# Kernel tuning notes

Measured on AMD Instinct MI355X. Metric: run time of the kernel, lower is better.

## Reference

```python
import jax, jax.numpy as jnp
import numpy as np

N_NODES = 50000
N_EDGES = 800000
D = 128
N_LAYERS = 6  # nbaselayer=3 -> branches of depth 1,2,3
NBASELAYER = 3
BN_EPS = 1e-5


def setup_inputs() -> dict:
    key = jax.random.key(0)
    ks = jax.random.split(key, 11)
    stdv = 1.0 / np.sqrt(D)
    return {
        "x": jax.random.normal(ks[0], (N_NODES, D), jnp.float32),
        "row": jax.random.randint(ks[1], (N_EDGES,), 0, N_NODES),
        "col": jax.random.randint(ks[2], (N_EDGES,), 0, N_NODES),
        "edge_weight": jax.random.uniform(ks[3], (N_EDGES,), jnp.float32),
        "W": jax.random.uniform(ks[4], (N_LAYERS, D, D), jnp.float32, -stdv, stdv),
        "SW": jax.random.uniform(ks[5], (N_LAYERS, D, D), jnp.float32, -stdv, stdv),
        "b": jax.random.uniform(ks[6], (N_LAYERS, D), jnp.float32, -stdv, stdv),
        "gamma": jax.random.uniform(ks[7], (N_LAYERS, D), jnp.float32, 0.5, 1.5),
        "beta": jax.random.normal(ks[8], (N_LAYERS, D), jnp.float32) * 0.1,
        "rmean": jax.random.normal(ks[9], (N_LAYERS, D), jnp.float32) * 0.1,
        "rvar": jax.random.uniform(ks[10], (N_LAYERS, D), jnp.float32, 0.5, 1.5),
    }


def reference(x, row, col, edge_weight, W, SW, b, gamma, beta, rmean, rvar):
    n = x.shape[0]

    def gcn(l, h):
        # dense GEMM: [N, D] @ [D, D]
        support = h @ W[l]
        # sparse aggregation (spmm): out[row] += w * support[col]
        msg = support[col] * edge_weight[:, None]  # [E, D]
        agg = jax.ops.segment_sum(msg, row, num_segments=n)
        # self-loop + bias
        out = agg + h @ SW[l] + b[l]
        # BatchNorm1d (eval mode: running stats)
        out = (out - rmean[l]) * jax.lax.rsqrt(rvar[l] + BN_EPS) * gamma[l] + beta[l]
        return jax.nn.relu(out)

    idx = 0
    for j in range(NBASELAYER):
        subx = x
        for _ in range(j + 1):
            # faithful to source: each inner layer consumes x (not subx)
            subx = gcn(idx, x)
            idx += 1
        x = x + subx  # aggrmethod='add'
    return x
```

## Files before the change

kernel.cpp:

```cpp
#include <hip/hip_runtime.h>

#define DD 128
#define NNODES 50000
#define NEDGES 800000
#define BN_EPS 1e-5f
#define NB1 ((NEDGES + 4095) / 4096)
#define NGROUPS ((NNODES + 255) / 256)

typedef float f32x4 __attribute__((ext_vector_type(4)));
typedef short bf16x8 __attribute__((ext_vector_type(8)));

__device__ __forceinline__ unsigned short f2bf(float f) {
    unsigned u = __float_as_uint(f);
    u = (u + 0x7FFFu + ((u >> 16) & 1u)) >> 16;
    return (unsigned short)u;
}
__device__ __forceinline__ float bf2f(unsigned short s) {
    return __uint_as_float((unsigned)s << 16);
}
__device__ __forceinline__ unsigned packbf(float a, float b) {
    return (unsigned)f2bf(a) | ((unsigned)f2bf(b) << 16);
}
__device__ __forceinline__ float lo_bf(unsigned u) { return __uint_as_float(u << 16); }
__device__ __forceinline__ float hi_bf(unsigned u) { return __uint_as_float(u & 0xFFFF0000u); }

__global__ __launch_bounds__(256) void count_convx_kernel(
    const int* __restrict__ row, int* __restrict__ pbase,
    const float* __restrict__ x, unsigned* __restrict__ h16u,
    int nedges, int npairs)
{
    const int bid = blockIdx.x;
    if (bid < NB1) {
        __shared__ int cnt[256];
        cnt[threadIdx.x] = 0;
        __syncthreads();
        const int estart = bid * 4096;
        const int eend = min(estart + 4096, nedges);
        for (int e = estart + threadIdx.x; e < eend; e += 256)
            atomicAdd(&cnt[row[e] >> 8], 1);
        __syncthreads();
        pbase[bid * 256 + threadIdx.x] = cnt[threadIdx.x];
    } else {
        int stride = (gridDim.x - NB1) * 256;
        for (int i = (bid - NB1) * 256 + threadIdx.x; i < npairs; i += stride) {
            float2 v = ((const float2*)x)[i];
            h16u[i] = packbf(v.x, v.y);
        }
    }
}

__global__ __launch_bounds__(256) void scanall_convwf_kernel(
    int* __restrict__ pbase, int* __restrict__ bktbase, int* __restrict__ rowptr,
    const float* __restrict__ W, const float* __restrict__ SW,
    unsigned short* __restrict__ Wf)
{
    if (blockIdx.x == 0) {
        __shared__ int buf[256];
        const int t = threadIdx.x;
        int s = 0;
#pragma unroll 4
        for (int blk = 0; blk < NB1; ++blk) {
            int tmp = pbase[blk * 256 + t];
            pbase[blk * 256 + t] = s;
            s += tmp;
        }
        const int v = s;
        buf[t] = v;
        __syncthreads();
#pragma unroll
        for (int off = 1; off < 256; off <<= 1) {
            int tv = (t >= off) ? buf[t - off] : 0;
            __syncthreads();
            buf[t] += tv;
            __syncthreads();
        }
        bktbase[t] = buf[t] - v;
        if (t == 255) bktbase[256] = buf[255];
        if (t == 0) rowptr[NNODES] = NEDGES;
        return;
    }
    int t = (blockIdx.x - 1) * 256 + threadIdx.x;
    if (t < 3 * 8 * 8 * 64) {
        int lane = t & 63;
        int nt   = (t >> 6) & 7;
        int ks   = (t >> 9) & 7;
        int li   = t >> 12;
        const int lmap[3] = {0, 2, 5};
        int l = lmap[li];
        int nn = nt * 16 + (lane & 15);
        unsigned short* dst = Wf + (((size_t)li * 64 + ks * 8 + nt) * 64 + lane) * 8;
#pragma unroll
        for (int i = 0; i < 8; ++i) {
            int k = ks * 32 + (lane >> 4) * 8 + i;
            float v = (k < 128) ? W[((size_t)l * 128 + k) * 128 + nn]
                                : SW[((size_t)l * 128 + (k - 128)) * 128 + nn];
            dst[i] = f2bf(v);
        }
    }
}

__global__ __launch_bounds__(256) void sort_pass1_kernel(
    const int* __restrict__ row, const int* __restrict__ col,
    const float* __restrict__ ew, const int* __restrict__ pbase,
    const int* __restrict__ bktbase, uint2* __restrict__ inter, int nedges)
{
    __shared__ int base[256];
    __shared__ int cnt[256];
    base[threadIdx.x] = pbase[blockIdx.x * 256 + threadIdx.x] + bktbase[threadIdx.x];
    cnt[threadIdx.x] = 0;
    __syncthreads();
    const int estart = blockIdx.x * 4096;
    const int eend = min(estart + 4096, nedges);
    for (int e = estart + threadIdx.x; e < eend; e += 256) {
        int r = row[e];
        int b = r >> 8;
        int k = atomicAdd(&cnt[b], 1);
        unsigned payload = (unsigned)col[e] | ((unsigned)f2bf(ew[e]) << 16);
        inter[base[b] + k] = make_uint2(payload, (unsigned)(r & 255));
    }
}

__global__ __launch_bounds__(256) void sort_pass2_kernel(
    const int* __restrict__ bktbase, const uint2* __restrict__ inter,
    int* __restrict__ rowptr, unsigned* __restrict__ cedge, int n)
{
    __shared__ int cnt[256];
    __shared__ int cur[256];
    const int g = blockIdx.x;
    const int rows0 = g * 256;
    const int jbeg = bktbase[g];
    const int jend = bktbase[g + 1];
    cnt[threadIdx.x] = 0;
    __syncthreads();
    for (int j = jbeg + threadIdx.x; j < jend; j += 256)
        atomicAdd(&cnt[inter[j].y], 1);
    __syncthreads();
    const int v = cnt[threadIdx.x];
    __syncthreads();
#pragma unroll
    for (int off = 1; off < 256; off <<= 1) {
        int t = (threadIdx.x >= off) ? cnt[threadIdx.x - off] : 0;
        __syncthreads();
        cnt[threadIdx.x] += t;
        __syncthreads();
    }
    const int rp = jbeg + cnt[threadIdx.x] - v;
    if (rows0 + threadIdx.x < n) rowptr[rows0 + threadIdx.x] = rp;
    cur[threadIdx.x] = rp;
    __syncthreads();
    for (int j = jbeg + threadIdx.x; j < jend; j += 256) {
        uint2 rec = inter[j];
        int p = atomicAdd(&cur[rec.y], 1);
        cedge[p] = rec.x;
    }
}

__global__ __launch_bounds__(256) void spmm_gather16_kernel(
    const uint4* __restrict__ h4, const int* __restrict__ rowptr,
    const unsigned* __restrict__ ce, uint4* __restrict__ agg4, int n)
{
    int node = blockIdx.x * 4 + (threadIdx.x >> 6);
    if (node >= n) return;
    const int lane = threadIdx.x & 63;
    const int q    = lane >> 4;
    const int l16  = lane & 15;
    const int beg = rowptr[node];
    const int end = rowptr[node + 1];

    float a0 = 0.f, a1 = 0.f, a2 = 0.f, a3 = 0.f;
    float a4 = 0.f, a5 = 0.f, a6 = 0.f, a7 = 0.f;

    int j = beg + q;
    for (; j + 12 < end; j += 16) {
        unsigned e0 = ce[j], e1 = ce[j+4], e2 = ce[j+8], e3 = ce[j+12];
        uint4 v0 = h4[(size_t)(e0 & 0xFFFFu) * 16 + l16];
        uint4 v1 = h4[(size_t)(e1 & 0xFFFFu) * 16 + l16];
        uint4 v2 = h4[(size_t)(e2 & 0xFFFFu) * 16 + l16];
        uint4 v3 = h4[(size_t)(e3 & 0xFFFFu) * 16 + l16];
        float w0 = bf2f((unsigned short)(e0 >> 16));
        float w1 = bf2f((unsigned short)(e1 >> 16));
        float w2 = bf2f((unsigned short)(e2 >> 16));
        float w3 = bf2f((unsigned short)(e3 >> 16));
        a0 += w0*lo_bf(v0.x) + w1*lo_bf(v1.x) + w2*lo_bf(v2.x) + w3*lo_bf(v3.x);
        a1 += w0*hi_bf(v0.x) + w1*hi_bf(v1.x) + w2*hi_bf(v2.x) + w3*hi_bf(v3.x);
        a2 += w0*lo_bf(v0.y) + w1*lo_bf(v1.y) + w2*lo_bf(v2.y) + w3*lo_bf(v3.y);
        a3 += w0*hi_bf(v0.y) + w1*hi_bf(v1.y) + w2*hi_bf(v2.y) + w3*hi_bf(v3.y);
        a4 += w0*lo_bf(v0.z) + w1*lo_bf(v1.z) + w2*lo_bf(v2.z) + w3*lo_bf(v3.z);
        a5 += w0*hi_bf(v0.z) + w1*hi_bf(v1.z) + w2*hi_bf(v2.z) + w3*hi_bf(v3.z);
        a6 += w0*lo_bf(v0.w) + w1*lo_bf(v1.w) + w2*lo_bf(v2.w) + w3*lo_bf(v3.w);
        a7 += w0*hi_bf(v0.w) + w1*hi_bf(v1.w) + w2*hi_bf(v2.w) + w3*hi_bf(v3.w);
    }
    for (; j < end; j += 4) {
        unsigned e = ce[j];
        uint4 v = h4[(size_t)(e & 0xFFFFu) * 16 + l16];
        float w = bf2f((unsigned short)(e >> 16));
        a0 += w * lo_bf(v.x); a1 += w * hi_bf(v.x);
        a2 += w * lo_bf(v.y); a3 += w * hi_bf(v.y);
        a4 += w * lo_bf(v.z); a5 += w * hi_bf(v.z);
        a6 += w * lo_bf(v.w); a7 += w * hi_bf(v.w);
    }
#pragma unroll
    for (int off = 16; off <= 32; off <<= 1) {
        a0 += __shfl_xor(a0, off); a1 += __shfl_xor(a1, off);
        a2 += __shfl_xor(a2, off); a3 += __shfl_xor(a3, off);
        a4 += __shfl_xor(a4, off); a5 += __shfl_xor(a5, off);
        a6 += __shfl_xor(a6, off); a7 += __shfl_xor(a7, off);
    }
    if (q == 0)
        agg4[(size_t)node * 16 + l16] =
            make_uint4(packbf(a0, a1), packbf(a2, a3), packbf(a4, a5), packbf(a6, a7));
}

__global__ __launch_bounds__(256) void gemm_mfma_kernel(
    unsigned short* __restrict__ h16,
    const unsigned short* __restrict__ agg16,
    const unsigned short* __restrict__ Wf,
    const float* __restrict__ bl, const float* __restrict__ gammal,
    const float* __restrict__ betal, const float* __restrict__ rmeanl,
    const float* __restrict__ rvarl,
    float* __restrict__ outf, int n, int write_f32)
{
    __shared__ __align__(16) unsigned short As[64 * 256];
    const int tid  = threadIdx.x;
    const int lane = tid & 63;
    const int wid  = tid >> 6;
    const int brow = blockIdx.x * 64;

    bf16x8 bfr[8][2];
#pragma unroll
    for (int ks = 0; ks < 8; ++ks)
#pragma unroll
        for (int nt2 = 0; nt2 < 2; ++nt2) {
            int nt = wid * 2 + nt2;
            bfr[ks][nt2] = *(const bf16x8*)(Wf + ((size_t)(ks * 8 + nt) * 64 + lane) * 8);
        }

#pragma unroll
    for (int it = 0; it < 8; ++it) {
        int id = tid + it * 256;
        int r  = id >> 5;
        int kc = id & 31;
        int grow = brow + r;
        uint4 v = make_uint4(0, 0, 0, 0);
        if (grow < n) {
            const unsigned short* src = (kc < 16)
                ? (agg16 + (size_t)grow * DD + kc * 8)
                : (h16   + (size_t)grow * DD + (kc - 16) * 8);
            v = *(const uint4*)src;
        }
        int kcs = kc ^ (r & 7);
        *(uint4*)(&As[r * 256 + kcs * 8]) = v;
    }
    __syncthreads();

    f32x4 acc[4][2];
#pragma unroll
    for (int i = 0; i < 4; ++i)
#pragma unroll
        for (int j = 0; j < 2; ++j)
            acc[i][j] = (f32x4){0.f, 0.f, 0.f, 0.f};

#pragma unroll
    for (int ks = 0; ks < 8; ++ks) {
#pragma unroll
        for (int mt = 0; mt < 4; ++mt) {
            int m   = mt * 16 + (lane & 15);
            int kc  = ks * 4 + (lane >> 4);
            int kcs = kc ^ (m & 7);
            bf16x8 afr = *(const bf16x8*)(&As[m * 256 + kcs * 8]);
            acc[mt][0] = __builtin_amdgcn_mfma_f32_16x16x32_bf16(afr, bfr[ks][0], acc[mt][0], 0, 0, 0);
            acc[mt][1] = __builtin_amdgcn_mfma_f32_16x16x32_bf16(afr, bfr[ks][1], acc[mt][1], 0, 0, 0);
        }
    }

#pragma unroll
    for (int nt2 = 0; nt2 < 2; ++nt2) {
        const int gcol = wid * 32 + nt2 * 16 + (lane & 15);
        const float sc = gammal[gcol] * __frsqrt_rn(rvarl[gcol] + BN_EPS);
        const float sh = (bl[gcol] - rmeanl[gcol]) * sc + betal[gcol];
        const int kc_res = 16 + (gcol >> 3);
        const int ko_res = gcol & 7;
#pragma unroll
        for (int mt = 0; mt < 4; ++mt) {
#pragma unroll
            for (int r = 0; r < 4; ++r) {
                int m = mt * 16 + (lane >> 4) * 4 + r;
                int grow = brow + m;
                if (grow < n) {
                    float res = bf2f(As[m * 256 + (kc_res ^ (m & 7)) * 8 + ko_res]);
                    float t = acc[mt][nt2][r] * sc + sh;
                    float o = res + (t > 0.f ? t : 0.f);
                    if (write_f32) outf[(size_t)grow * DD + gcol] = o;
                    else           h16[(size_t)grow * DD + gcol] = f2bf(o);
                }
            }
        }
    }
}

extern "C" void kernel_launch(void* const* d_in, const int* in_sizes, int n_in,
                              void* d_out, int out_size, void* d_ws, size_t ws_size,
                              hipStream_t stream) {
    const float* x     = (const float*)d_in[0];
    const int*   row   = (const int*)  d_in[1];
    const int*   col   = (const int*)  d_in[2];
    const float* ew    = (const float*)d_in[3];
    const float* W     = (const float*)d_in[4];
    const float* SW    = (const float*)d_in[5];
    const float* b     = (const float*)d_in[6];
    const float* gamma = (const float*)d_in[7];
    const float* beta  = (const float*)d_in[8];
    const float* rmean = (const float*)d_in[9];
    const float* rvar  = (const float*)d_in[10];

    float* out = (float*)d_out;

    char* ws = (char*)d_ws;
    unsigned*       agg16u = (unsigned*)ws;
    unsigned*       h16u   = (unsigned*)(ws + 12800000);
    unsigned short* Wf     = (unsigned short*)(ws + 25600000);
    int*   rowptr  = (int*)(ws + 25800000);
    int*   pbase   = (int*)(ws + 26010000);
    int*   bktbase = (int*)(ws + 26220000);
    unsigned* cedge = (unsigned*)(ws + 26400000);
    uint2*    inter = (uint2*)(ws + 29600000);

    count_convx_kernel<<<NB1 + 2048, 256, 0, stream>>>(
        row, pbase, x, h16u, NEDGES, NNODES * 64);
    scanall_convwf_kernel<<<1 + 48, 256, 0, stream>>>(
        pbase, bktbase, rowptr, W, SW, Wf);
    sort_pass1_kernel<<<NB1, 256, 0, stream>>>(
        row, col, ew, pbase, bktbase, inter, NEDGES);
    sort_pass2_kernel<<<NGROUPS, 256, 0, stream>>>(
        bktbase, inter, rowptr, cedge, NNODES);

    const int ggrid = (NNODES + 3) / 4;
    const int mgrid = (NNODES + 63) / 64;

    for (int li = 0; li < 3; ++li) {
        const int l = (li == 0) ? 0 : (li == 1) ? 2 : 5;
        spmm_gather16_kernel<<<ggrid, 256, 0, stream>>>(
            (const uint4*)h16u, rowptr, cedge, (uint4*)agg16u, NNODES);
        gemm_mfma_kernel<<<mgrid, 256, 0, stream>>>(
            (unsigned short*)h16u, (const unsigned short*)agg16u,
            Wf + (size_t)li * 32768,
            b + l * DD, gamma + l * DD, beta + l * DD, rmean + l * DD, rvar + l * DD,
            out, NNODES, li == 2 ? 1 : 0);
    }
}
```

Baseline: 186.7 us.

## Replace serial per-block bucket scan with atomic bucket counters; use direct global-to-LDS loads in GEMM

The bucket sort no longer stores per-block counts for a single-block serial scan. Counts are accumulated with global atomics, and sort_pass1 recounts its own chunk and claims bucket offsets atomically, which removes the long serial loop over all blocks in the scan kernel. The GEMM A-tile staging now uses global_load_lds to copy straight into shared memory with a pre-swizzled source address, skipping the register round trip, and is issued before the weight loads. Trade-offs: edge order within a bucket becomes nondeterministic, sort_pass1 reads row twice, out-of-range rows are left uninitialized in LDS, and an extra memset is added.

After: 187.1 us. Within noise of the previous version (+0.2%).

```diff
diff --git a/kernel.cpp b/kernel.cpp
--- a/kernel.cpp
+++ b/kernel.cpp
@@ -24,8 +24,14 @@
 __device__ __forceinline__ float lo_bf(unsigned u) { return __uint_as_float(u << 16); }
 __device__ __forceinline__ float hi_bf(unsigned u) { return __uint_as_float(u & 0xFFFF0000u); }
 
+__device__ __forceinline__ void gload_lds16(const void* g, void* l) {
+    __builtin_amdgcn_global_load_lds(
+        (const __attribute__((address_space(1))) unsigned int*)g,
+        (__attribute__((address_space(3))) unsigned int*)l, 16, 0, 0);
+}
+
 __global__ __launch_bounds__(256) void count_convx_kernel(
-    const int* __restrict__ row, int* __restrict__ pbase,
+    const int* __restrict__ row, int* __restrict__ bktcnt,
     const float* __restrict__ x, unsigned* __restrict__ h16u,
     int nedges, int npairs)
 {
@@ -39,7 +45,7 @@
         for (int e = estart + threadIdx.x; e < eend; e += 256)
             atomicAdd(&cnt[row[e] >> 8], 1);
         __syncthreads();
-        pbase[bid * 256 + threadIdx.x] = cnt[threadIdx.x];
+        if (cnt[threadIdx.x]) atomicAdd(&bktcnt[threadIdx.x], cnt[threadIdx.x]);
     } else {
         int stride = (gridDim.x - NB1) * 256;
         for (int i = (bid - NB1) * 256 + threadIdx.x; i < npairs; i += stride) {
@@ -50,21 +56,15 @@
 }
 
 __global__ __launch_bounds__(256) void scanall_convwf_kernel(
-    int* __restrict__ pbase, int* __restrict__ bktbase, int* __restrict__ rowptr,
+    const int* __restrict__ bktcnt, int* __restrict__ bktbase,
+    int* __restrict__ bcur, int* __restrict__ rowptr,
     const float* __restrict__ W, const float* __restrict__ SW,
     unsigned short* __restrict__ Wf)
 {
     if (blockIdx.x == 0) {
         __shared__ int buf[256];
         const int t = threadIdx.x;
-        int s = 0;
-#pragma unroll 4
-        for (int blk = 0; blk < NB1; ++blk) {
-            int tmp = pbase[blk * 256 + t];
-            pbase[blk * 256 + t] = s;
-            s += tmp;
-        }
-        const int v = s;
+        const int v = bktcnt[t];
         buf[t] = v;
         __syncthreads();
 #pragma unroll
@@ -74,7 +74,9 @@
             buf[t] += tv;
             __syncthreads();
         }
-        bktbase[t] = buf[t] - v;
+        const int excl = buf[t] - v;
+        bktbase[t] = excl;
+        bcur[t] = excl;
         if (t == 255) bktbase[256] = buf[255];
         if (t == 0) rowptr[NNODES] = NEDGES;
         return;
@@ -101,16 +103,23 @@
 
 __global__ __launch_bounds__(256) void sort_pass1_kernel(
     const int* __restrict__ row, const int* __restrict__ col,
-    const float* __restrict__ ew, const int* __restrict__ pbase,
-    const int* __restrict__ bktbase, uint2* __restrict__ inter, int nedges)
-{
+    const float* __restrict__ ew, int* __restrict__ bcur,
+    uint2* __restrict__ inter, int nedges)
+{
+    __shared__ int cnt[256];
     __shared__ int base[256];
-    __shared__ int cnt[256];
-    base[threadIdx.x] = pbase[blockIdx.x * 256 + threadIdx.x] + bktbase[threadIdx.x];
     cnt[threadIdx.x] = 0;
     __syncthreads();
     const int estart = blockIdx.x * 4096;
     const int eend = min(estart + 4096, nedges);
+    for (int e = estart + threadIdx.x; e < eend; e += 256)
+        atomicAdd(&cnt[row[e] >> 8], 1);
+    __syncthreads();
+    base[threadIdx.x] = cnt[threadIdx.x]
+        ? atomicAdd(&bcur[threadIdx.x], cnt[threadIdx.x]) : 0;
+    __syncthreads();
+    cnt[threadIdx.x] = 0;
+    __syncthreads();
     for (int e = estart + threadIdx.x; e < eend; e += 256) {
         int r = row[e];
         int b = r >> 8;
@@ -221,10 +230,26 @@
     float* __restrict__ outf, int n, int write_f32)
 {
     __shared__ __align__(16) unsigned short As[64 * 256];
-    const int tid  = threadIdx.x;
-    const int lane = tid & 63;
-    const int wid  = tid >> 6;
-    const int brow = blockIdx.x * 64;
+    const int tid   = threadIdx.x;
+    const int lane  = tid & 63;
+    const int wid   = tid >> 6;
+    const int wbase = tid & 192;
+    const int brow  = blockIdx.x * 64;
+
+#pragma unroll
+    for (int it = 0; it < 8; ++it) {
+        const int base_id = it * 256 + wbase;
+        const int id  = base_id + lane;
+        const int r   = id >> 5;
+        const int kc  = id & 31;
+        const int kcg = kc ^ (r & 7);
+        const int grow = brow + r;
+        const unsigned short* src = (kcg < 16)
+            ? (agg16 + (size_t)grow * DD + kcg * 8)
+            : (h16   + (size_t)grow * DD + (kcg - 16) * 8);
+        if (grow < n)
+            gload_lds16(src, &As[base_id * 8]);
+    }
 
     bf16x8 bfr[8][2];
 #pragma unroll
@@ -234,23 +259,6 @@
             int nt = wid * 2 + nt2;
             bfr[ks][nt2] = *(const bf16x8*)(Wf + ((size_t)(ks * 8 + nt) * 64 + lane) * 8);
         }
-
-#pragma unroll
-    for (int it = 0; it < 8; ++it) {
-        int id = tid + it * 256;
-        int r  = id >> 5;
-        int kc = id & 31;
-        int grow = brow + r;
-        uint4 v = make_uint4(0, 0, 0, 0);
-        if (grow < n) {
-            const unsigned short* src = (kc < 16)
-                ? (agg16 + (size_t)grow * DD + kc * 8)
-                : (h16   + (size_t)grow * DD + (kc - 16) * 8);
-            v = *(const uint4*)src;
-        }
-        int kcs = kc ^ (r & 7);
-        *(uint4*)(&As[r * 256 + kcs * 8]) = v;
-    }
     __syncthreads();
 
     f32x4 acc[4][2];
@@ -320,17 +328,19 @@
     unsigned*       h16u   = (unsigned*)(ws + 12800000);
     unsigned short* Wf     = (unsigned short*)(ws + 25600000);
     int*   rowptr  = (int*)(ws + 25800000);
-    int*   pbase   = (int*)(ws + 26010000);
-    int*   bktbase = (int*)(ws + 26220000);
+    int*   bktcnt  = (int*)(ws + 26010000);
+    int*   bktbase = (int*)(ws + 26011024);
+    int*   bcur    = (int*)(ws + 26012064);
     unsigned* cedge = (unsigned*)(ws + 26400000);
     uint2*    inter = (uint2*)(ws + 29600000);
 
+    hipMemsetAsync(bktcnt, 0, 256 * sizeof(int), stream);
     count_convx_kernel<<<NB1 + 2048, 256, 0, stream>>>(
-        row, pbase, x, h16u, NEDGES, NNODES * 64);
+        row, bktcnt, x, h16u, NEDGES, NNODES * 64);
     scanall_convwf_kernel<<<1 + 48, 256, 0, stream>>>(
-        pbase, bktbase, rowptr, W, SW, Wf);
+        bktcnt, bktbase, bcur, rowptr, W, SW, Wf);
     sort_pass1_kernel<<<NB1, 256, 0, stream>>>(
-        row, col, ew, pbase, bktbase, inter, NEDGES);
+        row, col, ew, bcur, inter, NEDGES);
     sort_pass2_kernel<<<NGROUPS, 256, 0, stream>>>(
         bktbase, inter, rowptr, cedge, NNODES);
 
```

## Fuse SpMM gather into MFMA GEMM layer kernel with ping-pong feature buffers

Applied to the files above, without the earlier changes.

Merges the separate sparse aggregation kernel and the dense MFMA GEMM into one per-layer kernel. Each block gathers neighbor features for its 64 rows straight into shared memory and loads the residual/self features with global_load_lds, so the aggregated tensor never round-trips through global memory. Feature buffers now ping-pong between two workspace regions. In exchange, each 16-lane group processes four nodes serially with a sequential 4-edge unroll instead of one node per wavefront, which lowers gather parallelism and may hurt latency hiding. The last block also loads rows past n via the unguarded LDS DMA.

Result: slower. 238.9 us (+28.0%).

```diff
diff --git a/kernel.cpp b/kernel.cpp
--- a/kernel.cpp
+++ b/kernel.cpp
@@ -6,6 +6,7 @@
 #define BN_EPS 1e-5f
 #define NB1 ((NEDGES + 4095) / 4096)
 #define NGROUPS ((NNODES + 255) / 256)
+#define NBLK_SCAN NGROUPS
 
 typedef float f32x4 __attribute__((ext_vector_type(4)));
 typedef short bf16x8 __attribute__((ext_vector_type(8)));
@@ -23,6 +24,12 @@
 }
 __device__ __forceinline__ float lo_bf(unsigned u) { return __uint_as_float(u << 16); }
 __device__ __forceinline__ float hi_bf(unsigned u) { return __uint_as_float(u & 0xFFFF0000u); }
+
+__device__ __forceinline__ void gload_lds16(const void* g, void* l) {
+    __builtin_amdgcn_global_load_lds(
+        (const __attribute__((address_space(1))) unsigned int*)g,
+        (__attribute__((address_space(3))) unsigned int*)l, 16, 0, 0);
+}
 
 __global__ __launch_bounds__(256) void count_convx_kernel(
     const int* __restrict__ row, int* __restrict__ pbase,
@@ -155,76 +162,83 @@
     }
 }
 
-__global__ __launch_bounds__(256) void spmm_gather16_kernel(
-    const uint4* __restrict__ h4, const int* __restrict__ rowptr,
-    const unsigned* __restrict__ ce, uint4* __restrict__ agg4, int n)
-{
-    int node = blockIdx.x * 4 + (threadIdx.x >> 6);
-    if (node >= n) return;
-    const int lane = threadIdx.x & 63;
-    const int q    = lane >> 4;
-    const int l16  = lane & 15;
-    const int beg = rowptr[node];
-    const int end = rowptr[node + 1];
-
-    float a0 = 0.f, a1 = 0.f, a2 = 0.f, a3 = 0.f;
-    float a4 = 0.f, a5 = 0.f, a6 = 0.f, a7 = 0.f;
-
-    int j = beg + q;
-    for (; j + 12 < end; j += 16) {
-        unsigned e0 = ce[j], e1 = ce[j+4], e2 = ce[j+8], e3 = ce[j+12];
-        uint4 v0 = h4[(size_t)(e0 & 0xFFFFu) * 16 + l16];
-        uint4 v1 = h4[(size_t)(e1 & 0xFFFFu) * 16 + l16];
-        uint4 v2 = h4[(size_t)(e2 & 0xFFFFu) * 16 + l16];
-        uint4 v3 = h4[(size_t)(e3 & 0xFFFFu) * 16 + l16];
-        float w0 = bf2f((unsigned short)(e0 >> 16));
-        float w1 = bf2f((unsigned short)(e1 >> 16));
-        float w2 = bf2f((unsigned short)(e2 >> 16));
-        float w3 = bf2f((unsigned short)(e3 >> 16));
-        a0 += w0*lo_bf(v0.x) + w1*lo_bf(v1.x) + w2*lo_bf(v2.x) + w3*lo_bf(v3.x);
-        a1 += w0*hi_bf(v0.x) + w1*hi_bf(v1.x) + w2*hi_bf(v2.x) + w3*hi_bf(v3.x);
-        a2 += w0*lo_bf(v0.y) + w1*lo_bf(v1.y) + w2*lo_bf(v2.y) + w3*lo_bf(v3.y);
-        a3 += w0*hi_bf(v0.y) + w1*hi_bf(v1.y) + w2*hi_bf(v2.y) + w3*hi_bf(v3.y);
-        a4 += w0*lo_bf(v0.z) + w1*lo_bf(v1.z) + w2*lo_bf(v2.z) + w3*lo_bf(v3.z);
-        a5 += w0*hi_bf(v0.z) + w1*hi_bf(v1.z) + w2*hi_bf(v2.z) + w3*hi_bf(v3.z);
-        a6 += w0*lo_bf(v0.w) + w1*lo_bf(v1.w) + w2*lo_bf(v2.w) + w3*lo_bf(v3.w);
-        a7 += w0*hi_bf(v0.w) + w1*hi_bf(v1.w) + w2*hi_bf(v2.w) + w3*hi_bf(v3.w);
-    }
-    for (; j < end; j += 4) {
-        unsigned e = ce[j];
-        uint4 v = h4[(size_t)(e & 0xFFFFu) * 16 + l16];
-        float w = bf2f((unsigned short)(e >> 16));
-        a0 += w * lo_bf(v.x); a1 += w * hi_bf(v.x);
-        a2 += w * lo_bf(v.y); a3 += w * hi_bf(v.y);
-        a4 += w * lo_bf(v.z); a5 += w * hi_bf(v.z);
-        a6 += w * lo_bf(v.w); a7 += w * hi_bf(v.w);
-    }
-#pragma unroll
-    for (int off = 16; off <= 32; off <<= 1) {
-        a0 += __shfl_xor(a0, off); a1 += __shfl_xor(a1, off);
-        a2 += __shfl_xor(a2, off); a3 += __shfl_xor(a3, off);
-        a4 += __shfl_xor(a4, off); a5 += __shfl_xor(a5, off);
-        a6 += __shfl_xor(a6, off); a7 += __shfl_xor(a7, off);
-    }
-    if (q == 0)
-        agg4[(size_t)node * 16 + l16] =
-            make_uint4(packbf(a0, a1), packbf(a2, a3), packbf(a4, a5), packbf(a6, a7));
-}
-
-__global__ __launch_bounds__(256) void gemm_mfma_kernel(
-    unsigned short* __restrict__ h16,
-    const unsigned short* __restrict__ agg16,
+__global__ __launch_bounds__(256) void layer_fused_kernel(
+    const unsigned short* __restrict__ h_in,
+    unsigned short* __restrict__ h_out,
+    const int* __restrict__ rowptr,
+    const unsigned* __restrict__ ce,
     const unsigned short* __restrict__ Wf,
     const float* __restrict__ bl, const float* __restrict__ gammal,
     const float* __restrict__ betal, const float* __restrict__ rmeanl,
     const float* __restrict__ rvarl,
     float* __restrict__ outf, int n, int write_f32)
 {
-    __shared__ __align__(16) unsigned short As[64 * 256];
-    const int tid  = threadIdx.x;
-    const int lane = tid & 63;
-    const int wid  = tid >> 6;
-    const int brow = blockIdx.x * 64;
+    __shared__ __align__(16) unsigned short As_agg[64 * 128];
+    __shared__ __align__(16) unsigned short As_h[64 * 128];
+    const int tid   = threadIdx.x;
+    const int lane  = tid & 63;
+    const int wid   = tid >> 6;
+    const int wbase = tid & 192;
+    const int brow  = blockIdx.x * 64;
+
+#pragma unroll
+    for (int it = 0; it < 4; ++it) {
+        const int base_id = it * 256 + wbase;
+        const int id  = base_id + lane;
+        const int r   = id >> 4;
+        const int kcs = id & 15;
+        const int kc  = kcs ^ (r & 7);
+        const unsigned short* src = h_in + (size_t)(brow + r) * DD + kc * 8;
+        gload_lds16(src, &As_h[base_id * 8]);
+    }
+
+    {
+        const int Q   = wid * 4 + (lane >> 4);
+        const int l16 = lane & 15;
+        const uint4* __restrict__ h4 = (const uint4*)h_in;
+        for (int i = 0; i < 4; ++i) {
+            const int r = Q * 4 + i;
+            const int node = brow + r;
+            if (node < n) {
+                const int beg = rowptr[node];
+                const int end = rowptr[node + 1];
+                float a0 = 0.f, a1 = 0.f, a2 = 0.f, a3 = 0.f;
+                float a4 = 0.f, a5 = 0.f, a6 = 0.f, a7 = 0.f;
+                int j = beg;
+                for (; j + 3 < end; j += 4) {
+                    unsigned e0 = ce[j], e1 = ce[j+1], e2 = ce[j+2], e3 = ce[j+3];
+                    uint4 v0 = h4[(size_t)(e0 & 0xFFFFu) * 16 + l16];
+                    uint4 v1 = h4[(size_t)(e1 & 0xFFFFu) * 16 + l16];
+                    uint4 v2 = h4[(size_t)(e2 & 0xFFFFu) * 16 + l16];
+                    uint4 v3 = h4[(size_t)(e3 & 0xFFFFu) * 16 + l16];
+                    float w0 = bf2f((unsigned short)(e0 >> 16));
+                    float w1 = bf2f((unsigned short)(e1 >> 16));
+                    float w2 = bf2f((unsigned short)(e2 >> 16));
+                    float w3 = bf2f((unsigned short)(e3 >> 16));
+                    a0 += w0*lo_bf(v0.x) + w1*lo_bf(v1.x) + w2*lo_bf(v2.x) + w3*lo_bf(v3.x);
+                    a1 += w0*hi_bf(v0.x) + w1*hi_bf(v1.x) + w2*hi_bf(v2.x) + w3*hi_bf(v3.x);
+                    a2 += w0*lo_bf(v0.y) + w1*lo_bf(v1.y) + w2*lo_bf(v2.y) + w3*lo_bf(v3.y);
+                    a3 += w0*hi_bf(v0.y) + w1*hi_bf(v1.y) + w2*hi_bf(v2.y) + w3*hi_bf(v3.y);
+                    a4 += w0*lo_bf(v0.z) + w1*lo_bf(v1.z) + w2*lo_bf(v2.z) + w3*lo_bf(v3.z);
+                    a5 += w0*hi_bf(v0.z) + w1*hi_bf(v1.z) + w2*hi_bf(v2.z) + w3*hi_bf(v3.z);
+                    a6 += w0*lo_bf(v0.w) + w1*lo_bf(v1.w) + w2*lo_bf(v2.w) + w3*lo_bf(v3.w);
+                    a7 += w0*hi_bf(v0.w) + w1*hi_bf(v1.w) + w2*hi_bf(v2.w) + w3*hi_bf(v3.w);
+                }
+                for (; j < end; ++j) {
+                    unsigned e = ce[j];
+                    uint4 v = h4[(size_t)(e & 0xFFFFu) * 16 + l16];
+                    float w = bf2f((unsigned short)(e >> 16));
+                    a0 += w * lo_bf(v.x); a1 += w * hi_bf(v.x);
+                    a2 += w * lo_bf(v.y); a3 += w * hi_bf(v.y);
+                    a4 += w * lo_bf(v.z); a5 += w * hi_bf(v.z);
+                    a6 += w * lo_bf(v.w); a7 += w * hi_bf(v.w);
+                }
+                *(uint4*)&As_agg[r * 128 + ((l16 ^ (r & 7)) << 3)] =
+                    make_uint4(packbf(a0, a1), packbf(a2, a3),
+                               packbf(a4, a5), packbf(a6, a7));
+            }
+        }
+    }
 
     bf16x8 bfr[8][2];
 #pragma unroll
@@ -234,23 +248,6 @@
             int nt = wid * 2 + nt2;
             bfr[ks][nt2] = *(const bf16x8*)(Wf + ((size_t)(ks * 8 + nt) * 64 + lane) * 8);
         }
-
-#pragma unroll
-    for (int it = 0; it < 8; ++it) {
-        int id = tid + it * 256;
-        int r  = id >> 5;
-        int kc = id & 31;
-        int grow = brow + r;
-        uint4 v = make_uint4(0, 0, 0, 0);
-        if (grow < n) {
-            const unsigned short* src = (kc < 16)
-                ? (agg16 + (size_t)grow * DD + kc * 8)
-                : (h16   + (size_t)grow * DD + (kc - 16) * 8);
-            v = *(const uint4*)src;
-        }
-        int kcs = kc ^ (r & 7);
-        *(uint4*)(&As[r * 256 + kcs * 8]) = v;
-    }
     __syncthreads();
 
     f32x4 acc[4][2];
@@ -264,10 +261,11 @@
     for (int ks = 0; ks < 8; ++ks) {
 #pragma unroll
         for (int mt = 0; mt < 4; ++mt) {
-            int m   = mt * 16 + (lane & 15);
-            int kc  = ks * 4 + (lane >> 4);
+            int m  = mt * 16 + (lane & 15);
+            int kc = (ks & 3) * 4 + (lane >> 4);
             int kcs = kc ^ (m & 7);
-            bf16x8 afr = *(const bf16x8*)(&As[m * 256 + kcs * 8]);
+            const unsigned short* Asrc = (ks < 4) ? As_agg : As_h;
+            bf16x8 afr = *(const bf16x8*)(&Asrc[m * 128 + (kcs << 3)]);
             acc[mt][0] = __builtin_amdgcn_mfma_f32_16x16x32_bf16(afr, bfr[ks][0], acc[mt][0], 0, 0, 0);
             acc[mt][1] = __builtin_amdgcn_mfma_f32_16x16x32_bf16(afr, bfr[ks][1], acc[mt][1], 0, 0, 0);
         }
@@ -278,7 +276,7 @@
         const int gcol = wid * 32 + nt2 * 16 + (lane & 15);
         const float sc = gammal[gcol] * __frsqrt_rn(rvarl[gcol] + BN_EPS);
         const float sh = (bl[gcol] - rmeanl[gcol]) * sc + betal[gcol];
-        const int kc_res = 16 + (gcol >> 3);
+        const int kc_res = gcol >> 3;
         const int ko_res = gcol & 7;
 #pragma unroll
         for (int mt = 0; mt < 4; ++mt) {
@@ -287,11 +285,11 @@
                 int m = mt * 16 + (lane >> 4) * 4 + r;
                 int grow = brow + m;
                 if (grow < n) {
-                    float res = bf2f(As[m * 256 + (kc_res ^ (m & 7)) * 8 + ko_res]);
+                    float res = bf2f(As_h[m * 128 + ((kc_res ^ (m & 7)) << 3) + ko_res]);
                     float t = acc[mt][nt2][r] * sc + sh;
                     float o = res + (t > 0.f ? t : 0.f);
                     if (write_f32) outf[(size_t)grow * DD + gcol] = o;
-                    else           h16[(size_t)grow * DD + gcol] = f2bf(o);
+                    else           h_out[(size_t)grow * DD + gcol] = f2bf(o);
                 }
             }
         }
@@ -316,9 +314,9 @@
     float* out = (float*)d_out;
 
     char* ws = (char*)d_ws;
-    unsigned*       agg16u = (unsigned*)ws;
-    unsigned*       h16u   = (unsigned*)(ws + 12800000);
-    unsigned short* Wf     = (unsigned short*)(ws + 25600000);
+    unsigned short* hA    = (unsigned short*)ws;
+    unsigned short* hB    = (unsigned short*)(ws + 12800000);
+    unsigned short* Wf    = (unsigned short*)(ws + 25600000);
     int*   rowptr  = (int*)(ws + 25800000);
     int*   pbase   = (int*)(ws + 26010000);
     int*   bktbase = (int*)(ws + 26220000);
@@ -326,7 +324,7 @@
     uint2*    inter = (uint2*)(ws + 29600000);
 
     count_convx_kernel<<<NB1 + 2048, 256, 0, stream>>>(
-        row, pbase, x, h16u, NEDGES, NNODES * 64);
+        row, pbase, x, (unsigned*)hA, NEDGES, NNODES * 64);
     scanall_convwf_kernel<<<1 + 48, 256, 0, stream>>>(
         pbase, bktbase, rowptr, W, SW, Wf);
     sort_pass1_kernel<<<NB1, 256, 0, stream>>>(
@@ -334,17 +332,17 @@
     sort_pass2_kernel<<<NGROUPS, 256, 0, stream>>>(
         bktbase, inter, rowptr, cedge, NNODES);
 
-    const int ggrid = (NNODES + 3) / 4;
     const int mgrid = (NNODES + 63) / 64;
 
+    const unsigned short* hin = hA;
+    unsigned short* hout = hB;
     for (int li = 0; li < 3; ++li) {
         const int l = (li == 0) ? 0 : (li == 1) ? 2 : 5;
-        spmm_gather16_kernel<<<ggrid, 256, 0, stream>>>(
-            (const uint4*)h16u, rowptr, cedge, (uint4*)agg16u, NNODES);
-        gemm_mfma_kernel<<<mgrid, 256, 0, stream>>>(
-            (unsigned short*)h16u, (const unsigned short*)agg16u,
+        layer_fused_kernel<<<mgrid, 256, 0, stream>>>(
+            hin, hout, rowptr, cedge,
             Wf + (size_t)li * 32768,
             b + l * DD, gamma + l * DD, beta + l * DD, rmean + l * DD, rvar + l * DD,
             out, NNODES, li == 2 ? 1 : 0);
-    }
-}
+        const unsigned short* t = hin; hin = hout; hout = (unsigned short*)t;
+    }
+}
```

## Balance SpMM edges across row groups and load GEMM tiles directly into LDS

Applied to the files above, without the earlier changes.

The per-node SpMM gather, where a 64-lane wave handled one node, is replaced by a kernel that takes a block of 32 rows and splits their combined edge range evenly across 16 lane groups. Each group finds its starting row by binary search, accumulates runs of edges, and flushes partial sums into a shared-memory fp32 accumulator with LDS atomics. This is meant to fix load imbalance from varying node degrees and idle lanes on low-degree nodes, at the cost of shared-memory atomics and a flush step. Separately, the GEMM A-tile staging now uses global_load_lds with the swizzle applied on the source side, skipping the register round trip. Out-of-range rows are no longer zero-filled.

Measured after the change: 279.1 us. 1.49x slower.

```diff
diff --git a/kernel.cpp b/kernel.cpp
--- a/kernel.cpp
+++ b/kernel.cpp
@@ -6,6 +6,8 @@
 #define BN_EPS 1e-5f
 #define NB1 ((NEDGES + 4095) / 4096)
 #define NGROUPS ((NNODES + 255) / 256)
+#define GROWS 32
+#define NGB ((NNODES + GROWS - 1) / GROWS)
 
 typedef float f32x4 __attribute__((ext_vector_type(4)));
 typedef short bf16x8 __attribute__((ext_vector_type(8)));
@@ -23,6 +25,12 @@
 }
 __device__ __forceinline__ float lo_bf(unsigned u) { return __uint_as_float(u << 16); }
 __device__ __forceinline__ float hi_bf(unsigned u) { return __uint_as_float(u & 0xFFFF0000u); }
+
+__device__ __forceinline__ void gload_lds16(const void* g, void* l) {
+    __builtin_amdgcn_global_load_lds(
+        (const __attribute__((address_space(1))) unsigned int*)g,
+        (__attribute__((address_space(3))) unsigned int*)l, 16, 0, 0);
+}
 
 __global__ __launch_bounds__(256) void count_convx_kernel(
     const int* __restrict__ row, int* __restrict__ pbase,
@@ -155,60 +163,89 @@
     }
 }
 
-__global__ __launch_bounds__(256) void spmm_gather16_kernel(
+__global__ __launch_bounds__(256) void spmm_stream_kernel(
     const uint4* __restrict__ h4, const int* __restrict__ rowptr,
     const unsigned* __restrict__ ce, uint4* __restrict__ agg4, int n)
 {
-    int node = blockIdx.x * 4 + (threadIdx.x >> 6);
-    if (node >= n) return;
-    const int lane = threadIdx.x & 63;
-    const int q    = lane >> 4;
-    const int l16  = lane & 15;
-    const int beg = rowptr[node];
-    const int end = rowptr[node + 1];
-
-    float a0 = 0.f, a1 = 0.f, a2 = 0.f, a3 = 0.f;
-    float a4 = 0.f, a5 = 0.f, a6 = 0.f, a7 = 0.f;
-
-    int j = beg + q;
-    for (; j + 12 < end; j += 16) {
-        unsigned e0 = ce[j], e1 = ce[j+4], e2 = ce[j+8], e3 = ce[j+12];
-        uint4 v0 = h4[(size_t)(e0 & 0xFFFFu) * 16 + l16];
-        uint4 v1 = h4[(size_t)(e1 & 0xFFFFu) * 16 + l16];
-        uint4 v2 = h4[(size_t)(e2 & 0xFFFFu) * 16 + l16];
-        uint4 v3 = h4[(size_t)(e3 & 0xFFFFu) * 16 + l16];
-        float w0 = bf2f((unsigned short)(e0 >> 16));
-        float w1 = bf2f((unsigned short)(e1 >> 16));
-        float w2 = bf2f((unsigned short)(e2 >> 16));
-        float w3 = bf2f((unsigned short)(e3 >> 16));
-        a0 += w0*lo_bf(v0.x) + w1*lo_bf(v1.x) + w2*lo_bf(v2.x) + w3*lo_bf(v3.x);
-        a1 += w0*hi_bf(v0.x) + w1*hi_bf(v1.x) + w2*hi_bf(v2.x) + w3*hi_bf(v3.x);
-        a2 += w0*lo_bf(v0.y) + w1*lo_bf(v1.y) + w2*lo_bf(v2.y) + w3*lo_bf(v3.y);
-        a3 += w0*hi_bf(v0.y) + w1*hi_bf(v1.y) + w2*hi_bf(v2.y) + w3*hi_bf(v3.y);
-        a4 += w0*lo_bf(v0.z) + w1*lo_bf(v1.z) + w2*lo_bf(v2.z) + w3*lo_bf(v3.z);
-        a5 += w0*hi_bf(v0.z) + w1*hi_bf(v1.z) + w2*hi_bf(v2.z) + w3*hi_bf(v3.z);
-        a6 += w0*lo_bf(v0.w) + w1*lo_bf(v1.w) + w2*lo_bf(v2.w) + w3*lo_bf(v3.w);
-        a7 += w0*hi_bf(v0.w) + w1*hi_bf(v1.w) + w2*hi_bf(v2.w) + w3*hi_bf(v3.w);
-    }
-    for (; j < end; j += 4) {
-        unsigned e = ce[j];
-        uint4 v = h4[(size_t)(e & 0xFFFFu) * 16 + l16];
-        float w = bf2f((unsigned short)(e >> 16));
-        a0 += w * lo_bf(v.x); a1 += w * hi_bf(v.x);
-        a2 += w * lo_bf(v.y); a3 += w * hi_bf(v.y);
-        a4 += w * lo_bf(v.z); a5 += w * hi_bf(v.z);
-        a6 += w * lo_bf(v.w); a7 += w * hi_bf(v.w);
-    }
-#pragma unroll
-    for (int off = 16; off <= 32; off <<= 1) {
-        a0 += __shfl_xor(a0, off); a1 += __shfl_xor(a1, off);
-        a2 += __shfl_xor(a2, off); a3 += __shfl_xor(a3, off);
-        a4 += __shfl_xor(a4, off); a5 += __shfl_xor(a5, off);
-        a6 += __shfl_xor(a6, off); a7 += __shfl_xor(a7, off);
-    }
-    if (q == 0)
-        agg4[(size_t)node * 16 + l16] =
-            make_uint4(packbf(a0, a1), packbf(a2, a3), packbf(a4, a5), packbf(a6, a7));
+    __shared__ float accf[GROWS][128];
+    __shared__ int rp[GROWS + 1];
+    const int tid  = threadIdx.x;
+    const int row0 = blockIdx.x * GROWS;
+    if (tid <= GROWS) rp[tid] = rowptr[min(row0 + tid, n)];
+    {
+        float* a = &accf[0][0];
+        for (int i = tid; i < GROWS * 128; i += 256) a[i] = 0.f;
+    }
+    __syncthreads();
+
+    const int q   = tid >> 4;
+    const int l16 = tid & 15;
+    const int jb = rp[0], T = rp[GROWS] - jb;
+    int j = jb + (T * q) / 16;
+    const int jend = jb + (T * (q + 1)) / 16;
+
+    if (j < jend) {
+        int lo = 0, hi = GROWS;
+        while (hi - lo > 1) { int mid = (lo + hi) >> 1; if (rp[mid] <= j) lo = mid; else hi = mid; }
+        int r = lo;
+        int nxt = rp[r + 1];
+        float a0=0.f,a1=0.f,a2=0.f,a3=0.f,a4=0.f,a5=0.f,a6=0.f,a7=0.f;
+        const int c0 = l16 * 8;
+
+#define FLUSH_RUN() do { \
+        atomicAdd(&accf[r][c0+0], a0); atomicAdd(&accf[r][c0+1], a1); \
+        atomicAdd(&accf[r][c0+2], a2); atomicAdd(&accf[r][c0+3], a3); \
+        atomicAdd(&accf[r][c0+4], a4); atomicAdd(&accf[r][c0+5], a5); \
+        atomicAdd(&accf[r][c0+6], a6); atomicAdd(&accf[r][c0+7], a7); \
+        a0=a1=a2=a3=a4=a5=a6=a7=0.f; } while (0)
+
+#define ACCUM(E, V) do { \
+        float w = bf2f((unsigned short)((E) >> 16)); \
+        a0 += w * lo_bf((V).x); a1 += w * hi_bf((V).x); \
+        a2 += w * lo_bf((V).y); a3 += w * hi_bf((V).y); \
+        a4 += w * lo_bf((V).z); a5 += w * hi_bf((V).z); \
+        a6 += w * lo_bf((V).w); a7 += w * hi_bf((V).w); } while (0)
+
+        while (j + 3 < jend) {
+            unsigned e0 = ce[j], e1 = ce[j+1], e2 = ce[j+2], e3 = ce[j+3];
+            uint4 v0 = h4[(size_t)(e0 & 0xFFFFu) * 16 + l16];
+            uint4 v1 = h4[(size_t)(e1 & 0xFFFFu) * 16 + l16];
+            uint4 v2 = h4[(size_t)(e2 & 0xFFFFu) * 16 + l16];
+            uint4 v3 = h4[(size_t)(e3 & 0xFFFFu) * 16 + l16];
+            while (j     >= nxt) { FLUSH_RUN(); ++r; nxt = rp[r+1]; }
+            ACCUM(e0, v0);
+            while (j + 1 >= nxt) { FLUSH_RUN(); ++r; nxt = rp[r+1]; }
+            ACCUM(e1, v1);
+            while (j + 2 >= nxt) { FLUSH_RUN(); ++r; nxt = rp[r+1]; }
+            ACCUM(e2, v2);
+            while (j + 3 >= nxt) { FLUSH_RUN(); ++r; nxt = rp[r+1]; }
+            ACCUM(e3, v3);
+            j += 4;
+        }
+        for (; j < jend; ++j) {
+            unsigned e = ce[j];
+            uint4 v = h4[(size_t)(e & 0xFFFFu) * 16 + l16];
+            while (j >= nxt) { FLUSH_RUN(); ++r; nxt = rp[r+1]; }
+            ACCUM(e, v);
+        }
+        FLUSH_RUN();
+#undef FLUSH_RUN
+#undef ACCUM
+    }
+    __syncthreads();
+
+#pragma unroll
+    for (int k = 0; k < 2; ++k) {
+        const int rr = q * 2 + k;
+        const int grow = row0 + rr;
+        if (grow < n) {
+            const float* ar = accf[rr];
+            const int c0 = l16 * 8;
+            agg4[(size_t)grow * 16 + l16] =
+                make_uint4(packbf(ar[c0+0], ar[c0+1]), packbf(ar[c0+2], ar[c0+3]),
+                           packbf(ar[c0+4], ar[c0+5]), packbf(ar[c0+6], ar[c0+7]));
+        }
+    }
 }
 
 __global__ __launch_bounds__(256) void gemm_mfma_kernel(
@@ -221,10 +258,26 @@
     float* __restrict__ outf, int n, int write_f32)
 {
     __shared__ __align__(16) unsigned short As[64 * 256];
-    const int tid  = threadIdx.x;
-    const int lane = tid & 63;
-    const int wid  = tid >> 6;
-    const int brow = blockIdx.x * 64;
+    const int tid   = threadIdx.x;
+    const int lane  = tid & 63;
+    const int wid   = tid >> 6;
+    const int wbase = tid & 192;
+    const int brow  = blockIdx.x * 64;
+
+#pragma unroll
+    for (int it = 0; it < 8; ++it) {
+        const int base_id = it * 256 + wbase;
+        const int id  = base_id + lane;
+        const int r   = id >> 5;
+        const int kc  = id & 31;
+        const int kcg = kc ^ (r & 7);
+        const int grow = brow + r;
+        const unsigned short* src = (kcg < 16)
+            ? (agg16 + (size_t)grow * DD + kcg * 8)
+            : (h16   + (size_t)grow * DD + (kcg - 16) * 8);
+        if (grow < n)
+            gload_lds16(src, &As[base_id * 8]);
+    }
 
     bf16x8 bfr[8][2];
 #pragma unroll
@@ -234,23 +287,6 @@
             int nt = wid * 2 + nt2;
             bfr[ks][nt2] = *(const bf16x8*)(Wf + ((size_t)(ks * 8 + nt) * 64 + lane) * 8);
         }
-
-#pragma unroll
-    for (int it = 0; it < 8; ++it) {
-        int id = tid + it * 256;
-        int r  = id >> 5;
-        int kc = id & 31;
-        int grow = brow + r;
-        uint4 v = make_uint4(0, 0, 0, 0);
-        if (grow < n) {
-            const unsigned short* src = (kc < 16)
-                ? (agg16 + (size_t)grow * DD + kc * 8)
-                : (h16   + (size_t)grow * DD + (kc - 16) * 8);
-            v = *(const uint4*)src;
-        }
-        int kcs = kc ^ (r & 7);
-        *(uint4*)(&As[r * 256 + kcs * 8]) = v;
-    }
     __syncthreads();
 
     f32x4 acc[4][2];
@@ -334,12 +370,11 @@
     sort_pass2_kernel<<<NGROUPS, 256, 0, stream>>>(
         bktbase, inter, rowptr, cedge, NNODES);
 
-    const int ggrid = (NNODES + 3) / 4;
     const int mgrid = (NNODES + 63) / 64;
 
     for (int li = 0; li < 3; ++li) {
         const int l = (li == 0) ? 0 : (li == 1) ? 2 : 5;
-        spmm_gather16_kernel<<<ggrid, 256, 0, stream>>>(
+        spmm_stream_kernel<<<NGB, 256, 0, stream>>>(
             (const uint4*)h16u, rowptr, cedge, (uint4*)agg16u, NNODES);
         gemm_mfma_kernel<<<mgrid, 256, 0, stream>>>(
             (unsigned short*)h16u, (const unsigned short*)agg16u,
```
